# Kernel tuning notes

Hardware: AMD Instinct MI355X
Metric: run time of the kernel (lower is better)

The kernel has to match this reference:

```python
import jax, jax.numpy as jnp
import numpy as np

EPS = 1e-6

def _normalize(x, eps=1e-12):
    n = jnp.linalg.norm(x, axis=-1, keepdims=True)
    return x / jnp.maximum(n, eps)

def _gather_nodes(nodes, idx):
    # nodes [B,N,C], idx [B,N,K] -> [B,N,K,C]
    B = nodes.shape[0]
    return nodes[jnp.arange(B)[:, None, None], idx]

def _dist(X, top_k):
    dX = X[:, None, :, :] - X[:, :, None, :]          # [B,N,N,3]
    D = jnp.sqrt(jnp.sum(dX * dX, axis=-1) + EPS)      # [B,N,N]
    neg_vals, E_idx = jax.lax.top_k(-D, top_k)         # smallest distances
    return D, -neg_vals, E_idx

def _gs_dist(D):
    D_min, D_max, D_count = 0.0, 20.0, 15
    D_mu = jnp.linspace(D_min, D_max, D_count)         # [15]
    D_sigma = (D_max - D_min) / D_count
    return jnp.exp(-(((D[..., None] - D_mu) / D_sigma) ** 2))

def _pos_encodings(E_idx, num_embeddings=16):
    N = E_idx.shape[1]
    ii = jnp.arange(N, dtype=jnp.float32)[None, :, None]
    d = (E_idx.astype(jnp.float32) - ii)[..., None]    # [B,N,K,1]
    freq = jnp.exp(jnp.arange(0, num_embeddings, 2, dtype=jnp.float32)
                   * -(np.log(10000.0) / num_embeddings))  # [8]
    angles = d * freq                                   # [B,N,K,8]
    return jnp.concatenate([jnp.cos(angles), jnp.sin(angles)], axis=-1)

def _orientations_coarse(X, E_idx, eps=1e-6):
    dX = X[:, 1:, :] - X[:, :-1, :]
    U = _normalize(dX)
    u_2, u_1, u_0 = U[:, :-2], U[:, 1:-1], U[:, 2:]
    n_2 = _normalize(jnp.cross(u_2, u_1))
    n_1 = _normalize(jnp.cross(u_1, u_0))
    cosA = jnp.clip(-(u_1 * u_0).sum(-1), -1 + eps, 1 - eps)
    A = jnp.arccos(cosA)
    cosD = jnp.clip((n_2 * n_1).sum(-1), -1 + eps, 1 - eps)
    Dang = jnp.sign((u_2 * n_1).sum(-1)) * jnp.arccos(cosD)
    AD = jnp.stack([jnp.cos(A), jnp.sin(A) * jnp.cos(Dang), jnp.sin(A) * jnp.sin(Dang)], axis=2)
    AD = jnp.pad(AD, ((0, 0), (1, 2), (0, 0)))          # [B,N,3]
    o_1 = _normalize(u_2 - u_1)
    O = jnp.stack([o_1, n_2, jnp.cross(o_1, n_2)], axis=2)  # [B,N-3,3,3]
    O = O.reshape(O.shape[0], O.shape[1], 9)
    O = jnp.pad(O, ((0, 0), (1, 2), (0, 0)))            # [B,N,9]
    O_nb = _gather_nodes(O, E_idx)                      # [B,N,K,9]
    X_nb = _gather_nodes(X, E_idx)                      # [B,N,K,3]
    O3 = O.reshape(O.shape[0], O.shape[1], 3, 3)
    dXn = X_nb - X[:, :, None, :]                       # [B,N,K,3]
    dU = jnp.einsum('bnij,bnkj->bnki', O3, dXn)         # rotate into local frame
    dU = _normalize(dU)
    # NOTE: original also computes R = O^T @ O_nb and quaternions Q, but Q is
    # dead code (never returned); omitted here (jit would DCE it anyway).
    return AD, dU

def setup_inputs() -> dict:
    key = jax.random.key(0)
    coords = jax.random.normal(key, (2, 4096, 3), dtype=jnp.float32) * 10.0
    return {"coords": coords, "num_k": 30}

def reference(coords, num_k):
    D, D_neighbors, E_idx = _dist(coords, num_k)
    gs_d = _gs_dist(D_neighbors)
    pos_emb = _pos_encodings(E_idx)
    AD_features, O_features = _orientations_coarse(coords, E_idx)
    return pos_emb, AD_features, O_features, gs_d, D_neighbors, E_idx
```

## Files before the change

kernel.cpp:

```cpp
#include <hip/hip_runtime.h>
#include <hip/hip_bf16.h>

constexpr int B = 2;
constexpr int N = 4096;
constexpr int K = 30;
constexpr int ROWS_PER_BLK = 4;

constexpr size_t OFF_POS = 0;
constexpr size_t OFF_AD  = OFF_POS + (size_t)B * N * K * 16;
constexpr size_t OFF_O   = OFF_AD  + (size_t)B * N * 3;
constexpr size_t OFF_GS  = OFF_O   + (size_t)B * N * K * 3;
constexpr size_t OFF_DN  = OFF_GS  + (size_t)B * N * K * 15;
constexpr size_t OFF_E   = OFF_DN  + (size_t)B * N * K;

constexpr float BIGD = 1e30f;
constexpr unsigned int BIGJ = 0xFFFFFFFFu;

struct F3 { float x, y, z; };

template <bool ISBF16>
__device__ __forceinline__ float ldx(const void* __restrict__ X, int idx) {
  if constexpr (ISBF16) {
    return __bfloat162float(((const __hip_bfloat16*)X)[idx]);
  } else {
    return ((const float*)X)[idx];
  }
}

template <bool ISBF16>
__device__ __forceinline__ float dist_core(float px, float py, float pz,
                                           float xi, float yi, float zi) {
#pragma clang fp contract(off)
  const float dx = px - xi;
  const float dy = py - yi;
  const float dz = pz - zi;
  return sqrtf(((dx * dx + dy * dy) + dz * dz) + 1e-6f);
}

template <bool ISBF16>
__device__ __forceinline__ float distf(const void* __restrict__ Xb, int j,
                                       float xi, float yi, float zi) {
  float px, py, pz;
  if constexpr (ISBF16) {
    px = ldx<true>(Xb, j * 3 + 0);
    py = ldx<true>(Xb, j * 3 + 1);
    pz = ldx<true>(Xb, j * 3 + 2);
  } else {
    const F3 p = ((const F3*)Xb)[j];
    px = p.x; py = p.y; pz = p.z;
  }
  return dist_core<ISBF16>(px, py, pz, xi, yi, zi);
}

template <int CTRL>
__device__ __forceinline__ float dpp_min_f32(float v) {
  const int mv = __builtin_amdgcn_update_dpp(__float_as_int(BIGD), __float_as_int(v),
                                             CTRL, 0xF, 0xF, false);
  return fminf(__int_as_float(mv), v);
}
template <int CTRL>
__device__ __forceinline__ unsigned int dpp_min_u32(unsigned int v) {
  const unsigned int mv = (unsigned int)__builtin_amdgcn_update_dpp(
      (int)BIGJ, (int)v, CTRL, 0xF, 0xF, false);
  return mv < v ? mv : v;
}
__device__ __forceinline__ float wave_min_f32_bcast(float v) {
  v = dpp_min_f32<0x111>(v);
  v = dpp_min_f32<0x112>(v);
  v = dpp_min_f32<0x114>(v);
  v = dpp_min_f32<0x118>(v);
  v = dpp_min_f32<0x142>(v);
  v = dpp_min_f32<0x143>(v);
  return __int_as_float(__builtin_amdgcn_readlane(__float_as_int(v), 63));
}
__device__ __forceinline__ unsigned int wave_min_u32_bcast(unsigned int v) {
  v = dpp_min_u32<0x111>(v);
  v = dpp_min_u32<0x112>(v);
  v = dpp_min_u32<0x114>(v);
  v = dpp_min_u32<0x118>(v);
  v = dpp_min_u32<0x142>(v);
  v = dpp_min_u32<0x143>(v);
  return (unsigned int)__builtin_amdgcn_readlane((int)v, 63);
}

__device__ __forceinline__ void lex_argmin(float d0, int j0,
                                           float& dmin, unsigned int& jmin) {
  dmin = wave_min_f32_bcast(d0);
  const unsigned long long tie = __ballot(d0 == dmin);
  if (__popcll(tie) == 1) {
    const int wl = __ffsll((unsigned long long)tie) - 1;
    jmin = (unsigned int)__builtin_amdgcn_readlane(j0, wl);
  } else {
    const unsigned int jc = (d0 == dmin) ? (unsigned int)j0 : BIGJ;
    jmin = wave_min_u32_bcast(jc);
  }
}

__device__ __forceinline__ float red2pi(float x) {
  return x - 6.28318530718f * rintf(x * 0.15915494309f);
}

__device__ __forceinline__ void norm3(float& x, float& y, float& z) {
  float n = sqrtf((x * x + y * y) + z * z);
  n = fmaxf(n, 1e-12f);
  x /= n; y /= n; z /= n;
}

__device__ __forceinline__ void cross3(float ax, float ay, float az,
                                       float bx, float by, float bz,
                                       float& cx, float& cy, float& cz) {
  cx = ay * bz - az * by;
  cy = az * bx - ax * bz;
  cz = ax * by - ay * bx;
}

template <bool ISBF16>
__device__ __forceinline__ void body(const void* __restrict__ Xb,
                                     float* __restrict__ out,
                                     int b, int i, int lane) {
  const float xi = ldx<ISBF16>(Xb, i * 3 + 0);
  const float yi = ldx<ISBF16>(Xb, i * 3 + 1);
  const float zi = ldx<ISBF16>(Xb, i * 3 + 2);

  float d0 = BIGD, d1 = BIGD;
  int   j0 = 0x7FFFFFFF, j1 = 0x7FFFFFFF;
  if constexpr (!ISBF16) {
    const F3* __restrict__ P = ((const F3*)Xb) + lane;
#pragma unroll 8
    for (int t = 0; t < 64; ++t) {
      const F3 p = P[t * 64];
      const int j = t * 64 + lane;
      const float d = dist_core<ISBF16>(p.x, p.y, p.z, xi, yi, zi);
      const bool lt1 = d < d1;
      const float td = lt1 ? d : d1;
      const int   tj = lt1 ? j : j1;
      const bool lt0 = td < d0;
      d1 = lt0 ? d0 : td;  j1 = lt0 ? j0 : tj;
      d0 = lt0 ? td : d0;  j0 = lt0 ? tj : j0;
    }
  } else {
#pragma unroll 8
    for (int t = 0; t < 64; ++t) {
      const int j = t * 64 + lane;
      const float d = distf<ISBF16>(Xb, j, xi, yi, zi);
      const bool lt1 = d < d1;
      const float td = lt1 ? d : d1;
      const int   tj = lt1 ? j : j1;
      const bool lt0 = td < d0;
      d1 = lt0 ? d0 : td;  j1 = lt0 ? j0 : tj;
      d0 = lt0 ? td : d0;  j0 = lt0 ? tj : j0;
    }
  }

  unsigned long long exm = 0;
  int   sjv = 0;
  float sdv = 0.0f;
  for (int k = 0; k < K; ++k) {
    float dmin; unsigned int jmin;
    lex_argmin(d0, j0, dmin, jmin);
    if (lane == k) { sjv = (int)jmin; sdv = dmin; }

    const int w  = (int)(jmin & 63u);
    const int tw = (int)(jmin >> 6);
    if (lane == w) {
      exm |= (1ull << tw);
      d0 = d1; j0 = j1;
      d1 = BIGD; j1 = 0x7FFFFFFF;
    }
    if (__ballot(d0 == BIGD) != 0ull) {
      const unsigned int mlo = (unsigned int)__builtin_amdgcn_readlane((int)(unsigned int)(exm & 0xFFFFFFFFull), w);
      const unsigned int mhi = (unsigned int)__builtin_amdgcn_readlane((int)(unsigned int)(exm >> 32), w);
      const unsigned long long m = ((unsigned long long)mhi << 32) | mlo;
      const int j2 = (lane << 6) | w;
      const float d2 = distf<ISBF16>(Xb, j2, xi, yi, zi);
      const float dc = ((m >> lane) & 1ull) ? BIGD : d2;
      float dmin2; unsigned int jmin2;
      lex_argmin(dc, j2, dmin2, jmin2);
      if (lane == w) { d0 = dmin2; j0 = (int)jmin2; }
    }
  }

  float ad0 = 0.f, ad1 = 0.f, ad2 = 0.f;
  float o00 = 0.f, o01 = 0.f, o02 = 0.f;
  float o10 = 0.f, o11 = 0.f, o12 = 0.f;
  float o20 = 0.f, o21 = 0.f, o22 = 0.f;
  if (i >= 1 && i <= N - 3) {
    const float ax = ldx<ISBF16>(Xb, (i - 1) * 3 + 0), ay = ldx<ISBF16>(Xb, (i - 1) * 3 + 1), az = ldx<ISBF16>(Xb, (i - 1) * 3 + 2);
    const float cx = ldx<ISBF16>(Xb, (i + 1) * 3 + 0), cy = ldx<ISBF16>(Xb, (i + 1) * 3 + 1), cz = ldx<ISBF16>(Xb, (i + 1) * 3 + 2);
    const float ex = ldx<ISBF16>(Xb, (i + 2) * 3 + 0), ey = ldx<ISBF16>(Xb, (i + 2) * 3 + 1), ez = ldx<ISBF16>(Xb, (i + 2) * 3 + 2);
    float u2x = xi - ax, u2y = yi - ay, u2z = zi - az; norm3(u2x, u2y, u2z);
    float u1x = cx - xi, u1y = cy - yi, u1z = cz - zi; norm3(u1x, u1y, u1z);
    float u0x = ex - cx, u0y = ey - cy, u0z = ez - cz; norm3(u0x, u0y, u0z);
    float n2x, n2y, n2z; cross3(u2x, u2y, u2z, u1x, u1y, u1z, n2x, n2y, n2z); norm3(n2x, n2y, n2z);
    float n1x, n1y, n1z; cross3(u1x, u1y, u1z, u0x, u0y, u0z, n1x, n1y, n1z); norm3(n1x, n1y, n1z);
    const float dotu = (u1x * u0x + u1y * u0y) + u1z * u0z;
    const float cosA = fminf(fmaxf(-dotu, -1.0f + 1e-6f), 1.0f - 1e-6f);
    const float A = acosf(cosA);
    const float dotn = (n2x * n1x + n2y * n1y) + n2z * n1z;
    const float cosD = fminf(fmaxf(dotn, -1.0f + 1e-6f), 1.0f - 1e-6f);
    const float du2n1 = (u2x * n1x + u2y * n1y) + u2z * n1z;
    const float sg = (du2n1 > 0.f) ? 1.f : ((du2n1 < 0.f) ? -1.f : 0.f);
    const float Dang = sg * acosf(cosD);
    const float sA = __sinf(A),    cA = __cosf(A);
    const float sD = __sinf(Dang), cD = __cosf(Dang);
    ad0 = cA; ad1 = sA * cD; ad2 = sA * sD;
    float o1x = u2x - u1x, o1y = u2y - u1y, o1z = u2z - u1z; norm3(o1x, o1y, o1z);
    o00 = o1x; o01 = o1y; o02 = o1z;
    o10 = n2x; o11 = n2y; o12 = n2z;
    cross3(o1x, o1y, o1z, n2x, n2y, n2z, o20, o21, o22);
  }

  const int row = b * N + i;

  {
    const size_t base = OFF_POS + (size_t)row * (K * 16);
    const int p = lane & 15;
    const float fr = __expf((float)((p & 7) * 2) * -0.57564627f);
    const bool is_cos = (p < 8);
#pragma unroll
    for (int it = 0; it < 8; ++it) {
      const int idx = it * 64 + lane;
      const int k = (idx >> 4) < K ? (idx >> 4) : (K - 1);
      const int jk = __shfl(sjv, k, 64);
      const float df = (float)(jk - i);
      const float r = red2pi(df * fr);
      const float v = is_cos ? __cosf(r) : __sinf(r);
      if (idx < K * 16) out[base + idx] = v;
    }
  }

  {
    const size_t base = OFF_GS + (size_t)row * (K * 15);
#pragma unroll
    for (int it = 0; it < 8; ++it) {
      const int idx = it * 64 + lane;
      const int kq = idx / 15;
      const int k = kq < K ? kq : (K - 1);
      const int m = idx - kq * 15;
      const float d = __shfl(sdv, k, 64);
      const float mu = (float)(m * (20.0 / 14.0));
      const float q = (d - mu) / 1.3333334f;
      const float v = __expf(-(q * q));
      if (idx < K * 15) out[base + idx] = v;
    }
  }

  if (lane < K) {
    const size_t rowk = (size_t)row * K + lane;
    const int   j = sjv;
    out[OFF_E  + rowk] = (float)j;
    out[OFF_DN + rowk] = sdv;

    float px, py, pz;
    if constexpr (ISBF16) {
      px = ldx<true>(Xb, j * 3 + 0);
      py = ldx<true>(Xb, j * 3 + 1);
      pz = ldx<true>(Xb, j * 3 + 2);
    } else {
      const F3 p = ((const F3*)Xb)[j];
      px = p.x; py = p.y; pz = p.z;
    }
    const float gx = px - xi, gy = py - yi, gz = pz - zi;
    const float v0 = (o00 * gx + o01 * gy) + o02 * gz;
    const float v1 = (o10 * gx + o11 * gy) + o12 * gz;
    const float v2 = (o20 * gx + o21 * gy) + o22 * gz;
    const float nn = fmaxf(sqrtf((v0 * v0 + v1 * v1) + v2 * v2), 1e-12f);
    out[OFF_O + rowk * 3 + 0] = v0 / nn;
    out[OFF_O + rowk * 3 + 1] = v1 / nn;
    out[OFF_O + rowk * 3 + 2] = v2 / nn;
  } else if (lane < K + 3) {
    const int c = lane - K;
    const float v = (c == 0) ? ad0 : (c == 1) ? ad1 : ad2;
    out[OFF_AD + (size_t)row * 3 + c] = v;
  }
}

__global__ __launch_bounds__(64 * ROWS_PER_BLK)
void protein_feat_kernel(const void* __restrict__ X,
                         float* __restrict__ out) {
  const int lane = threadIdx.x & 63;
  const int wv   = threadIdx.x >> 6;
  const int row  = blockIdx.x * ROWS_PER_BLK + wv;
  const int b    = row >> 12;
  const int i    = row & (N - 1);

  const unsigned short h = ((const unsigned short*)X)[2 * lane];
  const int e = (h >> 7) & 0xFF;
  const bool sane = ((h & 0x7FFF) == 0) || (e >= 115 && e <= 134);
  const unsigned long long bal = __ballot(sane);
  const bool isbf16 = __popcll(bal) >= 40;

  if (isbf16) {
    const void* Xb = (const void*)((const __hip_bfloat16*)X + (size_t)b * N * 3);
    body<true>(Xb, out, b, i, lane);
  } else {
    const void* Xb = (const void*)((const float*)X + (size_t)b * N * 3);
    body<false>(Xb, out, b, i, lane);
  }
}

extern "C" void kernel_launch(void* const* d_in, const int* in_sizes, int n_in,
                              void* d_out, int out_size, void* d_ws, size_t ws_size,
                              hipStream_t stream) {
  const void* X = d_in[0];
  float* out = (float*)d_out;
  (void)in_sizes; (void)n_in; (void)d_ws; (void)ws_size; (void)out_size;
  protein_feat_kernel<<<dim3(B * N / ROWS_PER_BLK), dim3(64 * ROWS_PER_BLK), 0, stream>>>(X, out);
}
```

Measured before the change: 123.0 us.

## Process two query rows per wavefront to share coordinate loads and interleave selection

Each wavefront now handles two query rows (i and i+N/2) at once. Every loaded neighbor coordinate is used for two distance computations, and the two independent top-k selection chains are interleaved to expose more instruction-level parallelism. The grid shrinks to half as many blocks, so there are fewer wavefronts and more registers per wavefront, which may reduce occupancy and latency hiding.

```diff
diff --git a/kernel.cpp b/kernel.cpp
--- a/kernel.cpp
+++ b/kernel.cpp
@@ -4,7 +4,7 @@
 constexpr int B = 2;
 constexpr int N = 4096;
 constexpr int K = 30;
-constexpr int ROWS_PER_BLK = 4;
+constexpr int HALF = N / 2;
 
 constexpr size_t OFF_POS = 0;
 constexpr size_t OFF_AD  = OFF_POS + (size_t)B * N * K * 16;
@@ -27,7 +27,6 @@
   }
 }
 
-template <bool ISBF16>
 __device__ __forceinline__ float dist_core(float px, float py, float pz,
                                            float xi, float yi, float zi) {
 #pragma clang fp contract(off)
@@ -49,7 +48,7 @@
     const F3 p = ((const F3*)Xb)[j];
     px = p.x; py = p.y; pz = p.z;
   }
-  return dist_core<ISBF16>(px, py, pz, xi, yi, zi);
+  return dist_core(px, py, pz, xi, yi, zi);
 }
 
 template <int CTRL>
@@ -88,12 +87,27 @@
   dmin = wave_min_f32_bcast(d0);
   const unsigned long long tie = __ballot(d0 == dmin);
   if (__popcll(tie) == 1) {
-    const int wl = __ffsll((unsigned long long)tie) - 1;
+    const int wl = __ffsll(tie) - 1;
     jmin = (unsigned int)__builtin_amdgcn_readlane(j0, wl);
   } else {
-    const unsigned int jc = (d0 == dmin) ? (unsigned int)j0 : BIGJ;
-    jmin = wave_min_u32_bcast(jc);
-  }
+    jmin = wave_min_u32_bcast((d0 == dmin) ? (unsigned int)j0 : BIGJ);
+  }
+}
+
+template <bool ISBF16>
+__device__ __forceinline__ void refill(const void* __restrict__ Xb, int lane, int w,
+                                       unsigned long long exm,
+                                       float xi, float yi, float zi,
+                                       float& d0, int& j0) {
+  const unsigned int mlo = (unsigned int)__builtin_amdgcn_readlane((int)(unsigned int)(exm & 0xFFFFFFFFull), w);
+  const unsigned int mhi = (unsigned int)__builtin_amdgcn_readlane((int)(unsigned int)(exm >> 32), w);
+  const unsigned long long m = ((unsigned long long)mhi << 32) | mlo;
+  const int j2 = (lane << 6) | w;
+  const float d2 = distf<ISBF16>(Xb, j2, xi, yi, zi);
+  const float dc = ((m >> lane) & 1ull) ? BIGD : d2;
+  float dmin2; unsigned int jmin2;
+  lex_argmin(dc, j2, dmin2, jmin2);
+  if (lane == w) { d0 = dmin2; j0 = (int)jmin2; }
 }
 
 __device__ __forceinline__ float red2pi(float x) {
@@ -115,71 +129,11 @@
 }
 
 template <bool ISBF16>
-__device__ __forceinline__ void body(const void* __restrict__ Xb,
-                                     float* __restrict__ out,
-                                     int b, int i, int lane) {
-  const float xi = ldx<ISBF16>(Xb, i * 3 + 0);
-  const float yi = ldx<ISBF16>(Xb, i * 3 + 1);
-  const float zi = ldx<ISBF16>(Xb, i * 3 + 2);
-
-  float d0 = BIGD, d1 = BIGD;
-  int   j0 = 0x7FFFFFFF, j1 = 0x7FFFFFFF;
-  if constexpr (!ISBF16) {
-    const F3* __restrict__ P = ((const F3*)Xb) + lane;
-#pragma unroll 8
-    for (int t = 0; t < 64; ++t) {
-      const F3 p = P[t * 64];
-      const int j = t * 64 + lane;
-      const float d = dist_core<ISBF16>(p.x, p.y, p.z, xi, yi, zi);
-      const bool lt1 = d < d1;
-      const float td = lt1 ? d : d1;
-      const int   tj = lt1 ? j : j1;
-      const bool lt0 = td < d0;
-      d1 = lt0 ? d0 : td;  j1 = lt0 ? j0 : tj;
-      d0 = lt0 ? td : d0;  j0 = lt0 ? tj : j0;
-    }
-  } else {
-#pragma unroll 8
-    for (int t = 0; t < 64; ++t) {
-      const int j = t * 64 + lane;
-      const float d = distf<ISBF16>(Xb, j, xi, yi, zi);
-      const bool lt1 = d < d1;
-      const float td = lt1 ? d : d1;
-      const int   tj = lt1 ? j : j1;
-      const bool lt0 = td < d0;
-      d1 = lt0 ? d0 : td;  j1 = lt0 ? j0 : tj;
-      d0 = lt0 ? td : d0;  j0 = lt0 ? tj : j0;
-    }
-  }
-
-  unsigned long long exm = 0;
-  int   sjv = 0;
-  float sdv = 0.0f;
-  for (int k = 0; k < K; ++k) {
-    float dmin; unsigned int jmin;
-    lex_argmin(d0, j0, dmin, jmin);
-    if (lane == k) { sjv = (int)jmin; sdv = dmin; }
-
-    const int w  = (int)(jmin & 63u);
-    const int tw = (int)(jmin >> 6);
-    if (lane == w) {
-      exm |= (1ull << tw);
-      d0 = d1; j0 = j1;
-      d1 = BIGD; j1 = 0x7FFFFFFF;
-    }
-    if (__ballot(d0 == BIGD) != 0ull) {
-      const unsigned int mlo = (unsigned int)__builtin_amdgcn_readlane((int)(unsigned int)(exm & 0xFFFFFFFFull), w);
-      const unsigned int mhi = (unsigned int)__builtin_amdgcn_readlane((int)(unsigned int)(exm >> 32), w);
-      const unsigned long long m = ((unsigned long long)mhi << 32) | mlo;
-      const int j2 = (lane << 6) | w;
-      const float d2 = distf<ISBF16>(Xb, j2, xi, yi, zi);
-      const float dc = ((m >> lane) & 1ull) ? BIGD : d2;
-      float dmin2; unsigned int jmin2;
-      lex_argmin(dc, j2, dmin2, jmin2);
-      if (lane == w) { d0 = dmin2; j0 = (int)jmin2; }
-    }
-  }
-
+__device__ __forceinline__ void epilogue(const void* __restrict__ Xb,
+                                         float* __restrict__ out,
+                                         int b, int i, int lane,
+                                         int sjv, float sdv,
+                                         float xi, float yi, float zi) {
   float ad0 = 0.f, ad1 = 0.f, ad2 = 0.f;
   float o00 = 0.f, o01 = 0.f, o02 = 0.f;
   float o10 = 0.f, o11 = 0.f, o12 = 0.f;
@@ -247,7 +201,7 @@
 
   if (lane < K) {
     const size_t rowk = (size_t)row * K + lane;
-    const int   j = sjv;
+    const int j = sjv;
     out[OFF_E  + rowk] = (float)j;
     out[OFF_DN + rowk] = sdv;
 
@@ -275,14 +229,99 @@
   }
 }
 
-__global__ __launch_bounds__(64 * ROWS_PER_BLK)
+template <bool ISBF16>
+__device__ __forceinline__ void body(const void* __restrict__ Xb,
+                                     float* __restrict__ out,
+                                     int b, int iA, int iB, int lane) {
+  const float xiA = ldx<ISBF16>(Xb, iA * 3 + 0);
+  const float yiA = ldx<ISBF16>(Xb, iA * 3 + 1);
+  const float ziA = ldx<ISBF16>(Xb, iA * 3 + 2);
+  const float xiB = ldx<ISBF16>(Xb, iB * 3 + 0);
+  const float yiB = ldx<ISBF16>(Xb, iB * 3 + 1);
+  const float ziB = ldx<ISBF16>(Xb, iB * 3 + 2);
+
+  float d0A = BIGD, d1A = BIGD, d0B = BIGD, d1B = BIGD;
+  int   j0A = 0x7FFFFFFF, j1A = 0x7FFFFFFF, j0B = 0x7FFFFFFF, j1B = 0x7FFFFFFF;
+#pragma unroll 4
+  for (int t = 0; t < 64; ++t) {
+    const int j = t * 64 + lane;
+    float px, py, pz;
+    if constexpr (ISBF16) {
+      px = ldx<true>(Xb, j * 3 + 0);
+      py = ldx<true>(Xb, j * 3 + 1);
+      pz = ldx<true>(Xb, j * 3 + 2);
+    } else {
+      const F3 p = ((const F3*)Xb)[j];
+      px = p.x; py = p.y; pz = p.z;
+    }
+    const float dA = dist_core(px, py, pz, xiA, yiA, ziA);
+    const float dB = dist_core(px, py, pz, xiB, yiB, ziB);
+    {
+      const bool lt1 = dA < d1A;
+      const float td = lt1 ? dA : d1A;
+      const int   tj = lt1 ? j : j1A;
+      const bool lt0 = td < d0A;
+      d1A = lt0 ? d0A : td;  j1A = lt0 ? j0A : tj;
+      d0A = lt0 ? td : d0A;  j0A = lt0 ? tj : j0A;
+    }
+    {
+      const bool lt1 = dB < d1B;
+      const float td = lt1 ? dB : d1B;
+      const int   tj = lt1 ? j : j1B;
+      const bool lt0 = td < d0B;
+      d1B = lt0 ? d0B : td;  j1B = lt0 ? j0B : tj;
+      d0B = lt0 ? td : d0B;  j0B = lt0 ? tj : j0B;
+    }
+  }
+
+  unsigned long long exmA = 0, exmB = 0;
+  int   sjvA = 0, sjvB = 0;
+  float sdvA = 0.0f, sdvB = 0.0f;
+  for (int k = 0; k < K; ++k) {
+    const float dminA = wave_min_f32_bcast(d0A);
+    const float dminB = wave_min_f32_bcast(d0B);
+    const unsigned long long tieA = __ballot(d0A == dminA);
+    const unsigned long long tieB = __ballot(d0B == dminB);
+    unsigned int jminA, jminB;
+    if (__popcll(tieA) == 1) {
+      jminA = (unsigned int)__builtin_amdgcn_readlane(j0A, __ffsll(tieA) - 1);
+    } else {
+      jminA = wave_min_u32_bcast((d0A == dminA) ? (unsigned int)j0A : BIGJ);
+    }
+    if (__popcll(tieB) == 1) {
+      jminB = (unsigned int)__builtin_amdgcn_readlane(j0B, __ffsll(tieB) - 1);
+    } else {
+      jminB = wave_min_u32_bcast((d0B == dminB) ? (unsigned int)j0B : BIGJ);
+    }
+    if (lane == k) { sjvA = (int)jminA; sdvA = dminA; sjvB = (int)jminB; sdvB = dminB; }
+
+    const int wA = (int)(jminA & 63u), twA = (int)(jminA >> 6);
+    const int wB = (int)(jminB & 63u), twB = (int)(jminB >> 6);
+    if (lane == wA) { exmA |= (1ull << twA); d0A = d1A; j0A = j1A; d1A = BIGD; j1A = 0x7FFFFFFF; }
+    if (lane == wB) { exmB |= (1ull << twB); d0B = d1B; j0B = j1B; d1B = BIGD; j1B = 0x7FFFFFFF; }
+
+    const unsigned long long eA = __ballot(d0A == BIGD);
+    const unsigned long long eB = __ballot(d0B == BIGD);
+    if (eA | eB) {
+      if (eA) refill<ISBF16>(Xb, lane, wA, exmA, xiA, yiA, ziA, d0A, j0A);
+      if (eB) refill<ISBF16>(Xb, lane, wB, exmB, xiB, yiB, ziB, d0B, j0B);
+    }
+  }
+
+  epilogue<ISBF16>(Xb, out, b, iA, lane, sjvA, sdvA, xiA, yiA, ziA);
+  epilogue<ISBF16>(Xb, out, b, iB, lane, sjvB, sdvB, xiB, yiB, ziB);
+}
+
+__global__ __launch_bounds__(256)
 void protein_feat_kernel(const void* __restrict__ X,
                          float* __restrict__ out) {
   const int lane = threadIdx.x & 63;
   const int wv   = threadIdx.x >> 6;
-  const int row  = blockIdx.x * ROWS_PER_BLK + wv;
-  const int b    = row >> 12;
-  const int i    = row & (N - 1);
+  const int l    = blockIdx.x * 4 + wv;
+  const int b    = l >> 11;
+  const int i0   = l & (HALF - 1);
+  const int iA   = i0;
+  const int iB   = i0 + HALF;
 
   const unsigned short h = ((const unsigned short*)X)[2 * lane];
   const int e = (h >> 7) & 0xFF;
@@ -292,10 +331,10 @@
 
   if (isbf16) {
     const void* Xb = (const void*)((const __hip_bfloat16*)X + (size_t)b * N * 3);
-    body<true>(Xb, out, b, i, lane);
+    body<true>(Xb, out, b, iA, iB, lane);
   } else {
     const void* Xb = (const void*)((const float*)X + (size_t)b * N * 3);
-    body<false>(Xb, out, b, i, lane);
+    body<false>(Xb, out, b, iA, iB, lane);
   }
 }
 
@@ -305,5 +344,5 @@
   const void* X = d_in[0];
   float* out = (float*)d_out;
   (void)in_sizes; (void)n_in; (void)d_ws; (void)ws_size; (void)out_size;
-  protein_feat_kernel<<<dim3(B * N / ROWS_PER_BLK), dim3(64 * ROWS_PER_BLK), 0, stream>>>(X, out);
-}
+  protein_feat_kernel<<<dim3(B * HALF / 4), dim3(256), 0, stream>>>(X, out);
+}
```

Result: no change. 125.3 us (+1.8%).
